# Optimization experiments

Measured on AMD Instinct MI355X. Metric: run time of the kernel, lower is better.

The kernel has to match this reference:

```python
import jax, jax.numpy as jnp
import numpy as np

D_STATE = 16
D_CONV = 4


def _ln_cf(x, w, b, eps=1e-6):
    # channels_first LayerNorm over dim 1 of (B,C,H,W)
    u = x.mean(1, keepdims=True)
    s = ((x - u) ** 2).mean(1, keepdims=True)
    return w[:, None, None] * ((x - u) / jnp.sqrt(s + eps)) + b[:, None, None]


def _ln_last(x, w, b, eps=1e-5):
    u = x.mean(-1, keepdims=True)
    s = ((x - u) ** 2).mean(-1, keepdims=True)
    return (x - u) / jnp.sqrt(s + eps) * w + b


def _mamba(xn, Win, convw, convb, Wx, Wdt, bdt, Alog, Dp):
    # xn: (B, L, d_model); returns (B, L, d_inner) (out_proj is Identity in this module)
    B, L, _ = xn.shape
    di = Win.shape[0] // 2
    xz = xn @ Win.T                                   # (B,L,2*di), in_proj bias=False
    xc, z = xz[..., :di], xz[..., di:]
    # causal depthwise conv1d along L (pad left d_conv-1, slice == torch pad+trim)
    xt = jnp.pad(xc.transpose(0, 2, 1), ((0, 0), (0, 0), (D_CONV - 1, 0)))
    xt = jax.lax.conv_general_dilated(xt, convw[:, None, :], (1,), 'VALID',
                                      dimension_numbers=('NCH', 'OIH', 'NCH'),
                                      feature_group_count=di)
    xs = jax.nn.silu(xt + convb[None, :, None]).transpose(0, 2, 1)  # (B,L,di)
    dtr = Wdt.shape[1]
    x_dbl = xs @ Wx.T                                 # (B,L,dtr+2*ds)
    dt = x_dbl[..., :dtr]
    Bm = x_dbl[..., dtr:dtr + D_STATE]                # (B,L,ds)
    Cm = x_dbl[..., dtr + D_STATE:]                   # (B,L,ds)
    delta = jax.nn.softplus(dt @ Wdt.T + bdt)         # (B,L,di)
    A = -jnp.exp(Alog)                                # (di,ds)
    dA = jnp.exp(delta[..., None] * A)                # (B,L,di,ds)
    dBx = delta[..., None] * Bm[:, :, None, :] * xs[..., None]

    def step(h, ab):
        a, b2 = ab
        h = a * h + b2
        return h, h

    h0 = jnp.zeros((B, di, D_STATE), xn.dtype)
    _, hs = jax.lax.scan(step, h0, (dA.transpose(1, 0, 2, 3), dBx.transpose(1, 0, 2, 3)))
    y = jnp.einsum('lbds,bls->bld', hs, Cm) + xs * Dp
    return y * jax.nn.silu(z)


def _dwconv2d(u, k, dil):
    c = k.shape[0]
    return jax.lax.conv_general_dilated(u, k[:, None], (1, 1),
                                        [(dil, dil), (dil, dil)],
                                        rhs_dilation=(dil, dil),
                                        dimension_numbers=('NCHW', 'OIHW', 'NCHW'),
                                        feature_group_count=c)


def _block(x, gamma1, gamma2, ln1_w, ln1_b, mn_w, mn_b,
           f_Win, f_convw, f_convb, f_Wx, f_Wdt, f_bdt, f_Alog, f_D,
           b_Win, b_convw, b_convb, b_Wx, b_Wdt, b_bdt, b_Alog, b_D,
           Wout, msff_win, msff_dw1, msff_dw2, msff_dw3, msff_wout):
    B, C, H, W = x.shape
    L = H * W
    # --- BiPixelMambaLayer branch ---
    x1 = _ln_cf(x, ln1_w, ln1_b)                       # norm1 (channels_first)
    xf = x1.reshape(B, C, L).transpose(0, 2, 1)        # (B,L,C)
    xn = _ln_last(xf, mn_w, mn_b)                      # inner nn.LayerNorm (eps=1e-5)
    yf = _mamba(xn, f_Win, f_convw, f_convb, f_Wx, f_Wdt, f_bdt, f_Alog, f_D)
    yb = _mamba(xn[:, ::-1], b_Win, b_convw, b_convb, b_Wx, b_Wdt, b_bdt, b_Alog, b_D)
    yo = (yf + yb[:, ::-1]) @ Wout.T                   # shared out_proj (bias=False)
    x = x + gamma1[:, None, None] * (yo.transpose(0, 2, 1).reshape(B, C, H, W) + x1)
    # --- MSFF branch (norm1 reused) ---
    inp = x
    xm = _ln_cf(x, ln1_w, ln1_b)
    h = jnp.einsum('oc,bchw->bohw', msff_win, xm)      # project_in (1x1x1 conv, depth=1)
    hid = msff_dw1.shape[0]
    h1 = _dwconv2d(h[:, :hid], msff_dw1, 1)            # Conv3d 3x3x3 w/ depth=1 == 2D center slice
    h2 = _dwconv2d(h[:, hid:2 * hid], msff_dw2, 2)
    h3 = _dwconv2d(h[:, 2 * hid:], msff_dw3, 3)
    g = jax.nn.gelu(h1, approximate=False) * h2 * h3
    xm = jnp.einsum('oc,bchw->bohw', msff_wout, g)     # project_out
    return inp + gamma2[:, None, None] * xm


def setup_inputs() -> dict:
    key = jax.random.key(0)
    ks = jax.random.split(key, 40)
    dim, di, dtr, ds, hid, Bn, H, W = 96, 192, 6, 16, 192, 2, 64, 64
    r = lambda i, shape, s=0.05: jax.random.normal(ks[i], shape, jnp.float32) * s
    inp = {
        'x': r(0, (Bn, dim, H, W), 1.0),
        'gamma1': r(1, (dim,), 0.1), 'gamma2': r(2, (dim,), 0.1),
        'ln1_w': 1.0 + r(3, (dim,), 0.1), 'ln1_b': r(4, (dim,), 0.1),
        'mn_w': 1.0 + r(5, (dim,), 0.1), 'mn_b': r(6, (dim,), 0.1),
    }
    i = 7
    for p in ('f_', 'b_'):
        inp[p + 'Win'] = r(i, (2 * di, dim)); i += 1
        inp[p + 'convw'] = r(i, (di, D_CONV), 0.2); i += 1
        inp[p + 'convb'] = r(i, (di,), 0.1); i += 1
        inp[p + 'Wx'] = r(i, (dtr + 2 * ds, di)); i += 1
        inp[p + 'Wdt'] = r(i, (di, dtr), 0.1); i += 1
        inp[p + 'bdt'] = r(i, (di,), 0.1); i += 1
        inp[p + 'Alog'] = jax.random.uniform(ks[i], (di, ds), jnp.float32, 0.0, 2.5); i += 1
        inp[p + 'D'] = r(i, (di,), 0.5); i += 1
    inp['Wout'] = r(i, (dim, di)); i += 1
    inp['msff_win'] = r(i, (3 * hid, dim)); i += 1
    inp['msff_dw1'] = r(i, (hid, 3, 3), 0.2); i += 1
    inp['msff_dw2'] = r(i, (hid, 3, 3), 0.2); i += 1
    inp['msff_dw3'] = r(i, (hid, 3, 3), 0.2); i += 1
    inp['msff_wout'] = r(i, (dim, hid)); i += 1
    return inp


def reference(x, gamma1, gamma2, ln1_w, ln1_b, mn_w, mn_b,
              f_Win, f_convw, f_convb, f_Wx, f_Wdt, f_bdt, f_Alog, f_D,
              b_Win, b_convw, b_convb, b_Wx, b_Wdt, b_bdt, b_Alog, b_D,
              Wout, msff_win, msff_dw1, msff_dw2, msff_dw3, msff_wout):
    return _block(x, gamma1, gamma2, ln1_w, ln1_b, mn_w, mn_b,
                  f_Win, f_convw, f_convb, f_Wx, f_Wdt, f_bdt, f_Alog, f_D,
                  b_Win, b_convw, b_convb, b_Wx, b_Wdt, b_bdt, b_Alog, b_D,
                  Wout, msff_win, msff_dw1, msff_dw2, msff_dw3, msff_wout)
```

## Files before the change

### kernel.cpp

```cpp
#include <hip/hip_runtime.h>
#include <hip/hip_bf16.h>
#include <math.h>

typedef __hip_bfloat16 bf16;
typedef _Float16 f16;
typedef f16  f16x8  __attribute__((ext_vector_type(8)));
typedef short short8 __attribute__((ext_vector_type(8)));
typedef unsigned short ushort8 __attribute__((ext_vector_type(8)));
typedef float floatx4 __attribute__((ext_vector_type(4)));

#define L_SEQ 4096
#define BATCH 2
#define DIM   96
#define DI    192
#define DS    16
#define HID   192
#define NPOS  (BATCH * L_SEQ)
#define NCH   512
#define CHUNK 8
#define GRP   32
#define NGRP  (NCH / GRP)
#define NREC  (2 * BATCH * DI)
#define LDBL  40
#define LOG2E 1.44269504088896f
#define TP    32

__device__ __forceinline__ float silu_f(float x) { return x / (1.f + __expf(-x)); }
__device__ __forceinline__ float softplus_f(float x) {
    return fmaxf(x, 0.f) + __logf(1.f + __expf(-fabsf(x)));
}
__device__ __forceinline__ float b2f(bf16 v) { return __bfloat162float(v); }
__device__ __forceinline__ float us2f(unsigned short u) {
    union { unsigned int i; float f; } cv; cv.i = ((unsigned int)u) << 16; return cv.f;
}

__global__ void k_prep(const float* __restrict__ fWin, const float* __restrict__ bWin,
                       const float* __restrict__ fWx,  const float* __restrict__ bWx,
                       const float* __restrict__ Wout, const float* __restrict__ mwin,
                       const float* __restrict__ mwout,
                       const float* __restrict__ fAlog, const float* __restrict__ bAlog,
                       const float* __restrict__ mdw1, const float* __restrict__ mdw2,
                       const float* __restrict__ mdw3,
                       bf16* __restrict__ war, float* __restrict__ a2tab,
                       float* __restrict__ mdwt) {
    int i = blockIdx.x * blockDim.x + threadIdx.x;
    if (i < 180480) {
        float v;
        if (i < 36864)        v = fWin[i];
        else if (i < 73728)   v = bWin[i - 36864];
        else if (i < 81024)   v = fWx[i - 73728];
        else if (i < 88320)   v = bWx[i - 81024];
        else if (i < 106752)  v = Wout[i - 88320];
        else if (i < 162048)  v = mwin[i - 106752];
        else                  v = mwout[i - 162048];
        war[i] = __float2bfloat16(v);
    } else if (i < 186624) {
        int j = i - 180480;
        int dir = j / 3072, rem = j % 3072;
        const float* al = dir ? bAlog : fAlog;
        a2tab[j] = -__expf(al[rem]) * LOG2E;
    } else if (i < 191808) {
        int j = i - 186624;
        int cv = j / 1728, rem = j % 1728;
        int tap = rem / 192, c = rem % 192;
        const float* src = (cv == 0) ? mdw1 : (cv == 1) ? mdw2 : mdw3;
        mdwt[j] = src[c * 9 + tap];
    }
}

__global__ void k_ln12_t(const float* __restrict__ x,
                         const float* __restrict__ ln1w, const float* __restrict__ ln1b,
                         const float* __restrict__ mnw,  const float* __restrict__ mnb,
                         bf16* __restrict__ XNbf) {
    __shared__ float xt[DIM][TP + 1];
    __shared__ float rs[8][TP], rss[8][TP];
    __shared__ float uu[TP], rr[TP];
    int p0 = blockIdx.x * TP;
    int b = p0 >> 12, l0 = p0 & (L_SEQ - 1);
    int t = threadIdx.x;
    int tg = t >> 5, li = t & 31;

    for (int idx = t; idx < DIM * TP; idx += 256) {
        int c = idx >> 5, q = idx & 31;
        xt[c][q] = x[((size_t)(b * DIM + c)) * L_SEQ + l0 + q];
    }
    __syncthreads();
    {
        float s = 0.f, ss = 0.f;
        for (int c = tg; c < DIM; c += 8) { float v = xt[c][li]; s += v; ss += v * v; }
        rs[tg][li] = s; rss[tg][li] = ss;
    }
    __syncthreads();
    if (t < TP) {
        float s = 0.f, ss = 0.f;
#pragma unroll
        for (int g = 0; g < 8; g++) { s += rs[g][t]; ss += rss[g][t]; }
        float u = s / DIM;
        uu[t] = u; rr[t] = rsqrtf(ss / DIM - u * u + 1e-6f);
    }
    __syncthreads();
    {
        float u = uu[li], r = rr[li];
        float s2 = 0.f, ss2 = 0.f;
        for (int c = tg; c < DIM; c += 8) {
            float tv = ln1w[c] * (xt[c][li] - u) * r + ln1b[c];
            xt[c][li] = tv;
            s2 += tv; ss2 += tv * tv;
        }
        rs[tg][li] = s2; rss[tg][li] = ss2;
    }
    __syncthreads();
    if (t < TP) {
        float s = 0.f, ss = 0.f;
#pragma unroll
        for (int g = 0; g < 8; g++) { s += rs[g][t]; ss += rss[g][t]; }
        float u = s / DIM;
        uu[t] = u; rr[t] = rsqrtf(ss / DIM - u * u + 1e-5f);
    }
    __syncthreads();
    for (int idx = t; idx < DIM * TP; idx += 256) {
        int q = idx / DIM, c = idx % DIM;
        XNbf[(size_t)(p0 + q) * DIM + c] =
            __float2bfloat16((xt[c][q] - uu[q]) * rr[q] * mnw[c] + mnb[c]);
    }
}

__global__ void mfma_nt_dir(const bf16* __restrict__ A0, const bf16* __restrict__ A1,
                            const bf16* __restrict__ W0, const bf16* __restrict__ W1,
                            void* __restrict__ C0, void* __restrict__ C1,
                            int M, int N, int K, int ldc, int pad6, int obf) {
    int z = blockIdx.z;
    const bf16* A = z ? A1 : A0;
    const bf16* W = z ? W1 : W0;
    void* C = z ? C1 : C0;
    int wave = threadIdx.x >> 6, lane = threadIdx.x & 63;
    int m0 = blockIdx.x * 64 + wave * 16;
    int n0 = blockIdx.y * 64;
    int lm = lane & 15, quad = lane >> 4;
    const short* Ap = (const short*)A + (size_t)(m0 + lm) * K + quad * 8;
    const short* Wp = (const short*)W;
    floatx4 acc[4];
#pragma unroll
    for (int t = 0; t < 4; t++) acc[t] = (floatx4){0.f, 0.f, 0.f, 0.f};
    for (int k0 = 0; k0 < K; k0 += 32) {
        short8 a = *(const short8*)(Ap + k0);
#pragma unroll
        for (int t = 0; t < 4; t++) {
            int n = n0 + t * 16 + lm;
            short8 b = (n < N) ? *(const short8*)(Wp + (size_t)n * K + k0 + quad * 8)
                               : (short8){0,0,0,0,0,0,0,0};
            acc[t] = __builtin_amdgcn_mfma_f32_16x16x32_bf16(a, b, acc[t], 0, 0, 0);
        }
    }
#pragma unroll
    for (int t = 0; t < 4; t++) {
        int n = n0 + t * 16 + lm;
        if (n < N) {
            int nn = (pad6 && n >= 6) ? n + 2 : n;
#pragma unroll
            for (int r = 0; r < 4; r++) {
                int m = m0 + quad * 4 + r;
                if (obf) ((bf16*)C)[(size_t)m * ldc + nn] = __float2bfloat16(acc[t][r]);
                else     ((float*)C)[(size_t)m * ldc + nn] = acc[t][r];
            }
        }
    }
}

__global__ void mfma_nt(const bf16* __restrict__ A, const bf16* __restrict__ W,
                        bf16* __restrict__ C, int M, int N, int K, int ldc) {
    int wave = threadIdx.x >> 6, lane = threadIdx.x & 63;
    int m0 = blockIdx.x * 64 + wave * 16;
    int n0 = blockIdx.y * 64;
    int lm = lane & 15, quad = lane >> 4;
    const short* Ap = (const short*)A + (size_t)(m0 + lm) * K + quad * 8;
    const short* Wp = (const short*)W;
    floatx4 acc[4];
#pragma unroll
    for (int t = 0; t < 4; t++) acc[t] = (floatx4){0.f, 0.f, 0.f, 0.f};
    for (int k0 = 0; k0 < K; k0 += 32) {
        short8 a = *(const short8*)(Ap + k0);
#pragma unroll
        for (int t = 0; t < 4; t++) {
            int n = n0 + t * 16 + lm;
            short8 b = (n < N) ? *(const short8*)(Wp + (size_t)n * K + k0 + quad * 8)
                               : (short8){0,0,0,0,0,0,0,0};
            acc[t] = __builtin_amdgcn_mfma_f32_16x16x32_bf16(a, b, acc[t], 0, 0, 0);
        }
    }
#pragma unroll
    for (int t = 0; t < 4; t++) {
        int n = n0 + t * 16 + lm;
        if (n < N) {
#pragma unroll
            for (int r = 0; r < 4; r++) {
                int m = m0 + quad * 4 + r;
                C[(size_t)m * ldc + n] = __float2bfloat16(acc[t][r]);
            }
        }
    }
}

__global__ void mfma_out(const bf16* __restrict__ Y1, const bf16* __restrict__ Y2,
                         const bf16* __restrict__ W, float* __restrict__ C,
                         int M, int N, int K, int ldc) {
    int wave = threadIdx.x >> 6, lane = threadIdx.x & 63;
    int m0 = blockIdx.x * 64 + wave * 16;
    int n0 = blockIdx.y * 64;
    int lm = lane & 15, quad = lane >> 4;
    const short* A1p = (const short*)Y1 + (size_t)(m0 + lm) * K + quad * 8;
    const short* A2p = (const short*)Y2 + (size_t)(m0 + lm) * K + quad * 8;
    const short* Wp  = (const short*)W;
    floatx4 acc[4];
#pragma unroll
    for (int t = 0; t < 4; t++) acc[t] = (floatx4){0.f, 0.f, 0.f, 0.f};
    for (int k0 = 0; k0 < K; k0 += 32) {
        short8 a1 = *(const short8*)(A1p + k0);
        short8 a2 = *(const short8*)(A2p + k0);
#pragma unroll
        for (int t = 0; t < 4; t++) {
            int n = n0 + t * 16 + lm;
            short8 b = (n < N) ? *(const short8*)(Wp + (size_t)n * K + k0 + quad * 8)
                               : (short8){0,0,0,0,0,0,0,0};
            acc[t] = __builtin_amdgcn_mfma_f32_16x16x32_bf16(a1, b, acc[t], 0, 0, 0);
            acc[t] = __builtin_amdgcn_mfma_f32_16x16x32_bf16(a2, b, acc[t], 0, 0, 0);
        }
    }
#pragma unroll
    for (int t = 0; t < 4; t++) {
        int n = n0 + t * 16 + lm;
        if (n < N) {
#pragma unroll
            for (int r = 0; r < 4; r++) {
                int m = m0 + quad * 4 + r;
                C[(size_t)m * ldc + n] = acc[t][r];
            }
        }
    }
}

__global__ void mfma_msffout(const bf16* __restrict__ A, const bf16* __restrict__ Bm,
                             const float* __restrict__ XMID, const float* __restrict__ gamma2,
                             float* __restrict__ out, int M, int K) {
    int wave = threadIdx.x >> 6, lane = threadIdx.x & 63;
    int m0 = blockIdx.x * 64 + wave * 16;
    int n0 = blockIdx.y * 64;
    int lm = lane & 15, quad = lane >> 4;
    int am = m0 + lm;
    bool aval = am < M;
    const short* Ap = (const short*)A + (size_t)am * K + quad * 8;
    const short* Bp = (const short*)Bm;
    floatx4 acc[4];
#pragma unroll
    for (int t = 0; t < 4; t++) acc[t] = (floatx4){0.f, 0.f, 0.f, 0.f};
    for (int k0 = 0; k0 < K; k0 += 32) {
        short8 a = aval ? *(const short8*)(Ap + k0) : (short8){0,0,0,0,0,0,0,0};
#pragma unroll
        for (int t = 0; t < 4; t++) {
            int n = n0 + t * 16 + lm;
            short8 b = *(const short8*)(Bp + (size_t)n * K + k0 + quad * 8);
            acc[t] = __builtin_amdgcn_mfma_f32_16x16x32_bf16(a, b, acc[t], 0, 0, 0);
        }
    }
#pragma unroll
    for (int t = 0; t < 4; t++) {
        int n = n0 + t * 16 + lm;
        int b = n >> 12, l = n & (L_SEQ - 1);
#pragma unroll
        for (int r = 0; r < 4; r++) {
            int m = m0 + quad * 4 + r;
            if (m < M) {
                size_t idx = ((size_t)(b * M + m)) * L_SEQ + l;
                out[idx] = XMID[idx] + gamma2[m] * acc[t][r];
            }
        }
    }
}

__global__ void k_conv_v(const bf16* __restrict__ XZF, const bf16* __restrict__ XZB,
                         const float* __restrict__ fw, const float* __restrict__ fb,
                         const float* __restrict__ bw, const float* __restrict__ bb,
                         bf16* __restrict__ XSF, bf16* __restrict__ XSB) {
    int dirb = blockIdx.y;
    int i = blockIdx.x * blockDim.x + threadIdx.x;
    int dg = i % 24;
    int p = i / 24;
    int b = p >> 12, l = p & (L_SEQ - 1);
    int d0 = dg * 8;
    const bf16* XZ = dirb ? XZB : XZF;
    const float* cw = dirb ? bw : fw;
    const float* cb = dirb ? bb : fb;

    float4 w[8];
#pragma unroll
    for (int j = 0; j < 8; j++) w[j] = *(const float4*)(cw + (d0 + j) * 4);
    float acc[8];
#pragma unroll
    for (int j = 0; j < 8; j++) acc[j] = cb[d0 + j];

#pragma unroll
    for (int k = 0; k < 4; k++) {
        int ls = dirb ? (l + 3 - k) : (l - 3 + k);
        if (ls >= 0 && ls < L_SEQ) {
            ushort8 xv = *(const ushort8*)((const unsigned short*)XZ +
                           ((size_t)(b * L_SEQ + ls)) * 384 + d0);
#pragma unroll
            for (int j = 0; j < 8; j++) {
                float wk = (k == 0) ? w[j].x : (k == 1) ? w[j].y : (k == 2) ? w[j].z : w[j].w;
                acc[j] += wk * us2f(xv[j]);
            }
        }
    }
    ushort8 ov;
#pragma unroll
    for (int j = 0; j < 8; j++) {
        bf16 t = __float2bfloat16(silu_f(acc[j]));
        ov[j] = *(unsigned short*)&t;
    }
    *(ushort8*)((unsigned short*)(dirb ? XSB : XSF) + (size_t)p * DI + d0) = ov;
}

__global__ void k_scan_p1(const float* __restrict__ DBLF, const float* __restrict__ DBLB,
                          const bf16* __restrict__ XSF,  const bf16* __restrict__ XSB,
                          const float* __restrict__ fWdt, const float* __restrict__ fbdt,
                          const float* __restrict__ bWdt, const float* __restrict__ bbdt,
                          const float* __restrict__ a2tab,
                          f16* __restrict__ P, f16* __restrict__ Q) {
    int t = blockIdx.x * blockDim.x + threadIdx.x;
    int d = t % DI;
    int g = t / DI;
    int chunk = g & (NCH - 1);
    int dirb = g >> 9;
    int b = dirb & 1, dir = dirb >> 1;

    const float* DBL = dir ? DBLB : DBLF;
    const bf16*  XS  = dir ? XSB  : XSF;
    const float* wdt = (dir ? bWdt : fWdt) + d * 6;
    float bdtv = (dir ? bbdt : fbdt)[d];

    float wd[6];
#pragma unroll
    for (int r = 0; r < 6; r++) wd[r] = wdt[r];
    const float* a2p = a2tab + (dir * DI + d) * 16;
    float A2[16], h[16];
#pragma unroll
    for (int v = 0; v < 4; v++) {
        float4 a2v = *(const float4*)(a2p + 4 * v);
        A2[4*v] = a2v.x; A2[4*v+1] = a2v.y; A2[4*v+2] = a2v.z; A2[4*v+3] = a2v.w;
    }
#pragma unroll
    for (int s = 0; s < 16; s++) h[s] = 0.f;

    int l = dir ? (L_SEQ - 1 - chunk * CHUNK) : chunk * CHUNK;
    int stp = dir ? -1 : 1;
    float sumdel = 0.f;

    for (int i = 0; i < CHUNK; i++) {
        size_t p = (size_t)b * L_SEQ + l;
        const float* row = DBL + p * LDBL;
        float dtv = bdtv;
#pragma unroll
        for (int r = 0; r < 6; r++) dtv += row[r] * wd[r];
        float del = softplus_f(dtv);
        float xs  = b2f(XS[p * DI + d]);
        const float4* bm = (const float4*)(row + 8);
        float4 B0 = bm[0], B1 = bm[1], B2 = bm[2], B3 = bm[3];
        float Bm[16] = {B0.x,B0.y,B0.z,B0.w, B1.x,B1.y,B1.z,B1.w,
                        B2.x,B2.y,B2.z,B2.w, B3.x,B3.y,B3.z,B3.w};
        float dx = del * xs;
        sumdel += del;
#pragma unroll
        for (int s = 0; s < 16; s++) {
            float dA = exp2f(del * A2[s]);
            h[s] = dA * h[s] + dx * Bm[s];
        }
        l += stp;
    }
    size_t idx = ((size_t)g * DI + d) * 16;
    f16x8 q0, q1, p0, p1;
#pragma unroll
    for (int j = 0; j < 8; j++) {
        q0[j] = (f16)h[j];
        q1[j] = (f16)h[8 + j];
        p0[j] = (f16)exp2f(A2[j] * sumdel);
        p1[j] = (f16)exp2f(A2[8 + j] * sumdel);
    }
    *(f16x8*)(Q + idx)     = q0;
    *(f16x8*)(Q + idx + 8) = q1;
    *(f16x8*)(P + idx)     = p0;
    *(f16x8*)(P + idx + 8) = p1;
}

__global__ void k_scan_p2a(const f16* __restrict__ P, const f16* __restrict__ Q,
                           float* __restrict__ Pg, float* __restrict__ Qg) {
    int t = blockIdx.x * blockDim.x + threadIdx.x;
    int s8 = t & 1;
    int d = (t >> 1) % DI;
    int rest = t / (DI * 2);
    int grp = rest % NGRP;
    int dirb = rest / NGRP;

    float Pr[8], Qr[8];
#pragma unroll
    for (int j = 0; j < 8; j++) { Pr[j] = 1.f; Qr[j] = 0.f; }

    size_t base = (((size_t)(dirb * NCH + grp * GRP)) * DI + d) * 16 + s8 * 8;
    for (int i = 0; i < GRP; i++) {
        size_t idx = base + (size_t)i * (DI * 16);
        f16x8 p8 = *(const f16x8*)(P + idx);
        f16x8 q8 = *(const f16x8*)(Q + idx);
#pragma unroll
        for (int j = 0; j < 8; j++) {
            float pv = (float)p8[j], qv = (float)q8[j];
            Qr[j] = pv * Qr[j] + qv;
            Pr[j] *= pv;
        }
    }
    size_t gidx = (((size_t)(dirb * NGRP + grp)) * DI + d) * 16 + s8 * 8;
#pragma unroll
    for (int v = 0; v < 2; v++) {
        *(float4*)(Pg + gidx + 4 * v) = make_float4(Pr[4*v], Pr[4*v+1], Pr[4*v+2], Pr[4*v+3]);
        *(float4*)(Qg + gidx + 4 * v) = make_float4(Qr[4*v], Qr[4*v+1], Qr[4*v+2], Qr[4*v+3]);
    }
}

__global__ void k_scan_p2b(const float* __restrict__ Pg, float* __restrict__ Qg) {
    int u = blockIdx.x * blockDim.x + threadIdx.x;
    int s = u & 15;
    int dd = (u >> 4) % DI;
    int dirb = u / (DI * 16);
    float runQ = 0.f;
#pragma unroll
    for (int g = 0; g < NGRP; g++) {
        size_t i = (((size_t)(dirb * NGRP + g)) * DI + dd) * 16 + s;
        float pg = Pg[i], qg = Qg[i];
        Qg[i] = runQ;
        runQ = pg * runQ + qg;
    }
}

__global__ void k_scan_p2c(const f16* __restrict__ P, f16* __restrict__ Q,
                           const float* __restrict__ Qg) {
    int t = blockIdx.x * blockDim.x + threadIdx.x;
    int s8 = t & 1;
    int d = (t >> 1) % DI;
    int rest = t / (DI * 2);
    int grp = rest % NGRP;
    int dirb = rest / NGRP;

    size_t gidx = (((size_t)(dirb * NGRP + grp)) * DI + d) * 16 + s8 * 8;
    float runQ[8];
#pragma unroll
    for (int v = 0; v < 2; v++) {
        float4 qv = *(const float4*)(Qg + gidx + 4 * v);
        runQ[4*v] = qv.x; runQ[4*v+1] = qv.y; runQ[4*v+2] = qv.z; runQ[4*v+3] = qv.w;
    }

    size_t base = (((size_t)(dirb * NCH + grp * GRP)) * DI + d) * 16 + s8 * 8;
    for (int i = 0; i < GRP; i++) {
        size_t idx = base + (size_t)i * (DI * 16);
        f16x8 p8 = *(const f16x8*)(P + idx);
        f16x8 q8 = *(const f16x8*)(Q + idx);
        f16x8 o8;
#pragma unroll
        for (int j = 0; j < 8; j++) {
            o8[j] = (f16)runQ[j];
            runQ[j] = (float)p8[j] * runQ[j] + (float)q8[j];
        }
        *(f16x8*)(Q + idx) = o8;
    }
}

__global__ void k_scan_p3(const float* __restrict__ DBLF, const float* __restrict__ DBLB,
                          const bf16* __restrict__ XSF,  const bf16* __restrict__ XSB,
                          const bf16* __restrict__ XZF,  const bf16* __restrict__ XZB,
                          const float* __restrict__ fWdt, const float* __restrict__ fbdt,
                          const float* __restrict__ bWdt, const float* __restrict__ bbdt,
                          const float* __restrict__ a2tab,
                          const float* __restrict__ fD,    const float* __restrict__ bD,
                          const f16* __restrict__ Q,
                          bf16* __restrict__ YSF, bf16* __restrict__ YSB) {
    int t = blockIdx.x * blockDim.x + threadIdx.x;
    int d = t % DI;
    int g = t / DI;
    int chunk = g & (NCH - 1);
    int dirb = g >> 9;
    int b = dirb & 1, dir = dirb >> 1;

    const float* DBL = dir ? DBLB : DBLF;
    const bf16*  XS  = dir ? XSB  : XSF;
    const bf16*  XZ  = dir ? XZB  : XZF;
    const float* wdt = (dir ? bWdt : fWdt) + d * 6;
    float bdtv = (dir ? bbdt : fbdt)[d];
    float Dp = dir ? bD[d] : fD[d];
    bf16* Y = dir ? YSB : YSF;

    float wd[6];
#pragma unroll
    for (int r = 0; r < 6; r++) wd[r] = wdt[r];
    const float* a2p = a2tab + (dir * DI + d) * 16;
    float A2[16], h[16];
#pragma unroll
    for (int v = 0; v < 4; v++) {
        float4 a2v = *(const float4*)(a2p + 4 * v);
        A2[4*v] = a2v.x; A2[4*v+1] = a2v.y; A2[4*v+2] = a2v.z; A2[4*v+3] = a2v.w;
    }
    size_t idx = ((size_t)g * DI + d) * 16;
    f16x8 q0 = *(const f16x8*)(Q + idx);
    f16x8 q1 = *(const f16x8*)(Q + idx + 8);
#pragma unroll
    for (int j = 0; j < 8; j++) { h[j] = (float)q0[j]; h[8 + j] = (float)q1[j]; }

    int l = dir ? (L_SEQ - 1 - chunk * CHUNK) : chunk * CHUNK;
    int stp = dir ? -1 : 1;

    for (int i = 0; i < CHUNK; i++) {
        size_t p = (size_t)b * L_SEQ + l;
        const float* row = DBL + p * LDBL;
        float dtv = bdtv;
#pragma unroll
        for (int r = 0; r < 6; r++) dtv += row[r] * wd[r];
        float del = softplus_f(dtv);
        float xs  = b2f(XS[p * DI + d]);
        float z   = b2f(XZ[p * 384 + 192 + d]);
        const float4* bm = (const float4*)(row + 8);
        float4 B0 = bm[0], B1 = bm[1], B2 = bm[2], B3 = bm[3];
        float4 C0 = bm[4], C1 = bm[5], C2 = bm[6], C3 = bm[7];
        float Bm[16] = {B0.x,B0.y,B0.z,B0.w, B1.x,B1.y,B1.z,B1.w,
                        B2.x,B2.y,B2.z,B2.w, B3.x,B3.y,B3.z,B3.w};
        float Cm[16] = {C0.x,C0.y,C0.z,C0.w, C1.x,C1.y,C1.z,C1.w,
                        C2.x,C2.y,C2.z,C2.w, C3.x,C3.y,C3.z,C3.w};
        float dx = del * xs;
        float pr = 0.f;
#pragma unroll
        for (int s = 0; s < 16; s++) {
            float dA = exp2f(del * A2[s]);
            h[s] = dA * h[s] + dx * Bm[s];
            pr += h[s] * Cm[s];
        }
        Y[p * DI + d] = __float2bfloat16((pr + xs * Dp) * silu_f(z));
        l += stp;
    }
}

__global__ void k_mid_t(const float* __restrict__ x, const float* __restrict__ YO,
                        const float* __restrict__ gamma1,
                        const float* __restrict__ ln1w, const float* __restrict__ ln1b,
                        float* __restrict__ XMID, bf16* __restrict__ XM2cl) {
    __shared__ float xt[DIM][TP + 1];
    __shared__ float yt[DIM][TP + 1];
    __shared__ float rs[8][TP], rss[8][TP];
    __shared__ float uu[TP], rr[TP];
    int p0 = blockIdx.x * TP;
    int b = p0 >> 12, l0 = p0 & (L_SEQ - 1);
    int t = threadIdx.x;
    int tg = t >> 5, li = t & 31;

    for (int idx = t; idx < DIM * TP; idx += 256) {
        int c = idx >> 5, q = idx & 31;
        xt[c][q] = x[((size_t)(b * DIM + c)) * L_SEQ + l0 + q];
    }
    for (int idx = t; idx < DIM * TP; idx += 256) {
        int q = idx / DIM, c = idx % DIM;
        yt[c][q] = YO[(size_t)(p0 + q) * DIM + c];
    }
    __syncthreads();
    {
        float s = 0.f, ss = 0.f;
        for (int c = tg; c < DIM; c += 8) { float v = xt[c][li]; s += v; ss += v * v; }
        rs[tg][li] = s; rss[tg][li] = ss;
    }
    __syncthreads();
    if (t < TP) {
        float s = 0.f, ss = 0.f;
#pragma unroll
        for (int g = 0; g < 8; g++) { s += rs[g][t]; ss += rss[g][t]; }
        float u = s / DIM;
        uu[t] = u; rr[t] = rsqrtf(ss / DIM - u * u + 1e-6f);
    }
    __syncthreads();
    {
        float u = uu[li], r = rr[li];
        float s = 0.f, ss = 0.f;
        for (int c = tg; c < DIM; c += 8) {
            float xv = xt[c][li];
            float x1 = ln1w[c] * (xv - u) * r + ln1b[c];
            float v = xv + gamma1[c] * (yt[c][li] + x1);
            XMID[((size_t)(b * DIM + c)) * L_SEQ + l0 + li] = v;
            xt[c][li] = v;
            s += v; ss += v * v;
        }
        rs[tg][li] = s; rss[tg][li] = ss;
    }
    __syncthreads();
    if (t < TP) {
        float s = 0.f, ss = 0.f;
#pragma unroll
        for (int g = 0; g < 8; g++) { s += rs[g][t]; ss += rss[g][t]; }
        float u = s / DIM;
        uu[t] = u; rr[t] = rsqrtf(ss / DIM - u * u + 1e-6f);
    }
    __syncthreads();
    for (int idx = t; idx < DIM * TP; idx += 256) {
        int q = idx / DIM, c = idx % DIM;
        XM2cl[(size_t)(p0 + q) * DIM + c] =
            __float2bfloat16(ln1w[c] * (xt[c][q] - uu[q]) * rr[q] + ln1b[c]);
    }
}

__global__ void k_msff_v(const bf16* __restrict__ H, const float* __restrict__ mdwt,
                         bf16* __restrict__ G) {
    int i = blockIdx.x * blockDim.x + threadIdx.x;
    int cg = i % 24;
    int p = i / 24;
    int c0 = cg * 8;
    int b = p >> 12, l = p & (L_SEQ - 1);
    int y = l >> 6, xc = l & 63;
    float a1[8] = {}, a2[8] = {}, a3[8] = {};
    const unsigned short* Hu = (const unsigned short*)H;

#pragma unroll
    for (int ky = 0; ky < 3; ky++) {
#pragma unroll
        for (int kx = 0; kx < 3; kx++) {
            int tap = ky * 3 + kx;
            {
                int y1 = y + (ky - 1), x1 = xc + (kx - 1);
                if (y1 >= 0 && y1 < 64 && x1 >= 0 && x1 < 64) {
                    float4 w0 = *(const float4*)(mdwt + tap * 192 + c0);
                    float4 w1 = *(const float4*)(mdwt + tap * 192 + c0 + 4);
                    ushort8 hv = *(const ushort8*)(Hu +
                        ((size_t)(b * L_SEQ + y1 * 64 + x1)) * 576 + c0);
                    float wv[8] = {w0.x,w0.y,w0.z,w0.w, w1.x,w1.y,w1.z,w1.w};
#pragma unroll
                    for (int j = 0; j < 8; j++) a1[j] += wv[j] * us2f(hv[j]);
                }
            }
            {
                int y2 = y + (ky - 1) * 2, x2 = xc + (kx - 1) * 2;
                if (y2 >= 0 && y2 < 64 && x2 >= 0 && x2 < 64) {
                    float4 w0 = *(const float4*)(mdwt + (9 + tap) * 192 + c0);
                    float4 w1 = *(const float4*)(mdwt + (9 + tap) * 192 + c0 + 4);
                    ushort8 hv = *(const ushort8*)(Hu +
                        ((size_t)(b * L_SEQ + y2 * 64 + x2)) * 576 + 192 + c0);
                    float wv[8] = {w0.x,w0.y,w0.z,w0.w, w1.x,w1.y,w1.z,w1.w};
#pragma unroll
                    for (int j = 0; j < 8; j++) a2[j] += wv[j] * us2f(hv[j]);
                }
            }
            {
                int y3 = y + (ky - 1) * 3, x3 = xc + (kx - 1) * 3;
                if (y3 >= 0 && y3 < 64 && x3 >= 0 && x3 < 64) {
                    float4 w0 = *(const float4*)(mdwt + (18 + tap) * 192 + c0);
                    float4 w1 = *(const float4*)(mdwt + (18 + tap) * 192 + c0 + 4);
                    ushort8 hv = *(const ushort8*)(Hu +
                        ((size_t)(b * L_SEQ + y3 * 64 + x3)) * 576 + 384 + c0);
                    float wv[8] = {w0.x,w0.y,w0.z,w0.w, w1.x,w1.y,w1.z,w1.w};
#pragma unroll
                    for (int j = 0; j < 8; j++) a3[j] += wv[j] * us2f(hv[j]);
                }
            }
        }
    }
    ushort8 ov;
#pragma unroll
    for (int j = 0; j < 8; j++) {
        float ge = 0.5f * a1[j] * (1.f + erff(a1[j] * 0.70710678118f));
        bf16 t = __float2bfloat16(ge * a2[j] * a3[j]);
        ov[j] = *(unsigned short*)&t;
    }
    *(ushort8*)((unsigned short*)G + (size_t)p * HID + c0) = ov;
}

extern "C" void kernel_launch(void* const* d_in, const int* in_sizes, int n_in,
                              void* d_out, int out_size, void* d_ws, size_t ws_size,
                              hipStream_t stream) {
    const float* x      = (const float*)d_in[0];
    const float* gamma1 = (const float*)d_in[1];
    const float* gamma2 = (const float*)d_in[2];
    const float* ln1w   = (const float*)d_in[3];
    const float* ln1b   = (const float*)d_in[4];
    const float* mnw    = (const float*)d_in[5];
    const float* mnb    = (const float*)d_in[6];
    const float* fWin   = (const float*)d_in[7];
    const float* fconvw = (const float*)d_in[8];
    const float* fconvb = (const float*)d_in[9];
    const float* fWx    = (const float*)d_in[10];
    const float* fWdt   = (const float*)d_in[11];
    const float* fbdt   = (const float*)d_in[12];
    const float* fAlog  = (const float*)d_in[13];
    const float* fD     = (const float*)d_in[14];
    const float* bWin   = (const float*)d_in[15];
    const float* bconvw = (const float*)d_in[16];
    const float* bconvb = (const float*)d_in[17];
    const float* bWx    = (const float*)d_in[18];
    const float* bWdt   = (const float*)d_in[19];
    const float* bbdt   = (const float*)d_in[20];
    const float* bAlog  = (const float*)d_in[21];
    const float* bD     = (const float*)d_in[22];
    const float* Wout   = (const float*)d_in[23];
    const float* mwin   = (const float*)d_in[24];
    const float* mdw1   = (const float*)d_in[25];
    const float* mdw2   = (const float*)d_in[26];
    const float* mdw3   = (const float*)d_in[27];
    const float* mwout  = (const float*)d_in[28];
    float* out = (float*)d_out;

    float* ws = (float*)d_ws;
    bf16*  XNbf  = (bf16*)(ws);
    bf16*  XZF   = (bf16*)(ws + 393216);
    bf16*  XZB   = (bf16*)(ws + 1966080);
    bf16*  XSF   = (bf16*)(ws + 3538944);
    bf16*  XSB   = (bf16*)(ws + 4325376);
    float* DBLF  = ws + 5111808;
    float* DBLB  = ws + 5439488;
    f16*   Ph    = (f16*)(ws + 5767168);
    f16*   Qh    = (f16*)(ws + 8912896);
    bf16*  YSFbf = (bf16*)(ws + 12058624);
    bf16*  YSBbf = (bf16*)(ws + 12845056);
    float* YO    = ws + 13631488;
    float* XMID  = ws + 14417920;
    bf16*  XM2cl = (bf16*)(ws + 15204352);
    bf16*  Hcl   = (bf16*)(ws + 15597568);
    bf16*  Gcl   = (bf16*)(ws + 17956864);
    bf16*  WAR   = (bf16*)(ws + 18743296);
    float* A2tab = ws + 18833536;
    float* MDWT  = ws + 18839680;
    float* Pgb   = ws + 18844864;
    float* Qgb   = ws + 19041472;

    const bf16* fWinB  = WAR;
    const bf16* bWinB  = WAR + 36864;
    const bf16* fWxB   = WAR + 73728;
    const bf16* bWxB   = WAR + 81024;
    const bf16* WoutB  = WAR + 88320;
    const bf16* mwinB  = WAR + 106752;
    const bf16* mwoutB = WAR + 162048;

    k_prep<<<750, 256, 0, stream>>>(fWin, bWin, fWx, bWx, Wout, mwin, mwout,
                                    fAlog, bAlog, mdw1, mdw2, mdw3,
                                    WAR, A2tab, MDWT);
    k_ln12_t<<<NPOS / TP, 256, 0, stream>>>(x, ln1w, ln1b, mnw, mnb, XNbf);
    mfma_nt_dir<<<dim3(128, 6, 2), 256, 0, stream>>>(XNbf, XNbf, fWinB, bWinB,
                                                     XZF, XZB, NPOS, 384, DIM, 384, 0, 1);
    k_conv_v<<<dim3(NPOS * 24 / 256, 2), 256, 0, stream>>>(XZF, XZB, fconvw, fconvb,
                                                           bconvw, bconvb, XSF, XSB);
    mfma_nt_dir<<<dim3(128, 1, 2), 256, 0, stream>>>(XSF, XSB, fWxB, bWxB,
                                                     DBLF, DBLB, NPOS, 38, DI, LDBL, 1, 0);
    k_scan_p1<<<NREC * NCH / 256, 256, 0, stream>>>(DBLF, DBLB, XSF, XSB,
                                                    fWdt, fbdt, bWdt, bbdt,
                                                    A2tab, Ph, Qh);
    k_scan_p2a<<<4 * NGRP * DI * 2 / 256, 256, 0, stream>>>(Ph, Qh, Pgb, Qgb);
    k_scan_p2b<<<NREC * 16 / 256, 256, 0, stream>>>(Pgb, Qgb);
    k_scan_p2c<<<4 * NGRP * DI * 2 / 256, 256, 0, stream>>>(Ph, Qh, Qgb);
    k_scan_p3<<<NREC * NCH / 256, 256, 0, stream>>>(DBLF, DBLB, XSF, XSB, XZF, XZB,
                                                    fWdt, fbdt, bWdt, bbdt,
                                                    A2tab, fD, bD, Qh,
                                                    YSFbf, YSBbf);
    mfma_out<<<dim3(128, 2), 256, 0, stream>>>(YSFbf, YSBbf, WoutB, YO, NPOS, DIM, DI, DIM);
    k_mid_t<<<NPOS / TP, 256, 0, stream>>>(x, YO, gamma1, ln1w, ln1b, XMID, XM2cl);
    mfma_nt<<<dim3(128, 9), 256, 0, stream>>>(XM2cl, mwinB, Hcl, NPOS, 576, DIM, 576);
    k_msff_v<<<NPOS * 24 / 256, 256, 0, stream>>>(Hcl, MDWT, Gcl);
    mfma_msffout<<<dim3(2, 128), 256, 0, stream>>>(mwoutB, Gcl, XMID, gamma2, out, DIM, HID);
}
```

Baseline: 287.7 us.

## Fuse chunk scan with in-block group combine and merge prep into layernorm

The chunked selective scan is restructured: chunks become longer (16 steps, 256 chunks). Each block now combines its group of chunk summaries in shared memory and writes the exclusive prefix P/Q plus the group totals directly. This replaces the separate p2a and p2c passes. Phase 3 then rebuilds each chunk's initial state as Pexc*Qg+Qexc, and the weight-prep kernel is merged into the layernorm launch as extra blocks. The aim is fewer launches and less global round-tripping of chunk summaries, at the cost of longer serial chunks, reduced parallelism in p1/p3, and an extra f16 rounding of the exclusive products.

Result: faster. 269.6 us (-6.3%).

```diff
diff --git a/kernel.cpp b/kernel.cpp
--- a/kernel.cpp
+++ b/kernel.cpp
@@ -16,12 +16,13 @@
 #define DS    16
 #define HID   192
 #define NPOS  (BATCH * L_SEQ)
-#define NCH   512
-#define CHUNK 8
-#define GRP   32
+#define NCH   256
+#define CHUNK 16
+#define GRP   16
 #define NGRP  (NCH / GRP)
 #define NREC  (2 * BATCH * DI)
 #define LDBL  40
+#define PLANE (4 * NCH * DI * 8)
 #define LOG2E 1.44269504088896f
 #define TP    32
 
@@ -34,47 +35,48 @@
     union { unsigned int i; float f; } cv; cv.i = ((unsigned int)u) << 16; return cv.f;
 }
 
-__global__ void k_prep(const float* __restrict__ fWin, const float* __restrict__ bWin,
-                       const float* __restrict__ fWx,  const float* __restrict__ bWx,
-                       const float* __restrict__ Wout, const float* __restrict__ mwin,
-                       const float* __restrict__ mwout,
-                       const float* __restrict__ fAlog, const float* __restrict__ bAlog,
-                       const float* __restrict__ mdw1, const float* __restrict__ mdw2,
-                       const float* __restrict__ mdw3,
-                       bf16* __restrict__ war, float* __restrict__ a2tab,
-                       float* __restrict__ mdwt) {
-    int i = blockIdx.x * blockDim.x + threadIdx.x;
-    if (i < 180480) {
-        float v;
-        if (i < 36864)        v = fWin[i];
-        else if (i < 73728)   v = bWin[i - 36864];
-        else if (i < 81024)   v = fWx[i - 73728];
-        else if (i < 88320)   v = bWx[i - 81024];
-        else if (i < 106752)  v = Wout[i - 88320];
-        else if (i < 162048)  v = mwin[i - 106752];
-        else                  v = mwout[i - 162048];
-        war[i] = __float2bfloat16(v);
-    } else if (i < 186624) {
-        int j = i - 180480;
-        int dir = j / 3072, rem = j % 3072;
-        const float* al = dir ? bAlog : fAlog;
-        a2tab[j] = -__expf(al[rem]) * LOG2E;
-    } else if (i < 191808) {
-        int j = i - 186624;
-        int cv = j / 1728, rem = j % 1728;
-        int tap = rem / 192, c = rem % 192;
-        const float* src = (cv == 0) ? mdw1 : (cv == 1) ? mdw2 : mdw3;
-        mdwt[j] = src[c * 9 + tap];
-    }
-}
-
-__global__ void k_ln12_t(const float* __restrict__ x,
-                         const float* __restrict__ ln1w, const float* __restrict__ ln1b,
-                         const float* __restrict__ mnw,  const float* __restrict__ mnb,
-                         bf16* __restrict__ XNbf) {
+__global__ void k_ln12_prep(const float* __restrict__ x,
+                            const float* __restrict__ ln1w, const float* __restrict__ ln1b,
+                            const float* __restrict__ mnw,  const float* __restrict__ mnb,
+                            bf16* __restrict__ XNbf,
+                            const float* __restrict__ fWin, const float* __restrict__ bWin,
+                            const float* __restrict__ fWx,  const float* __restrict__ bWx,
+                            const float* __restrict__ Wout, const float* __restrict__ mwin,
+                            const float* __restrict__ mwout,
+                            const float* __restrict__ fAlog, const float* __restrict__ bAlog,
+                            const float* __restrict__ mdw1, const float* __restrict__ mdw2,
+                            const float* __restrict__ mdw3,
+                            bf16* __restrict__ war, float* __restrict__ a2tab,
+                            float* __restrict__ mdwt) {
     __shared__ float xt[DIM][TP + 1];
     __shared__ float rs[8][TP], rss[8][TP];
     __shared__ float uu[TP], rr[TP];
+    if (blockIdx.x >= NPOS / TP) {
+        int i = (blockIdx.x - NPOS / TP) * 256 + threadIdx.x;
+        if (i < 180480) {
+            float v;
+            if (i < 36864)        v = fWin[i];
+            else if (i < 73728)   v = bWin[i - 36864];
+            else if (i < 81024)   v = fWx[i - 73728];
+            else if (i < 88320)   v = bWx[i - 81024];
+            else if (i < 106752)  v = Wout[i - 88320];
+            else if (i < 162048)  v = mwin[i - 106752];
+            else                  v = mwout[i - 162048];
+            war[i] = __float2bfloat16(v);
+        } else if (i < 186624) {
+            int j = i - 180480;
+            int dir = j / 3072, rem = j % 3072;
+            const float* al = dir ? bAlog : fAlog;
+            a2tab[j] = -__expf(al[rem]) * LOG2E;
+        } else if (i < 191808) {
+            int j = i - 186624;
+            int cv = j / 1728, rem = j % 1728;
+            int tap = rem / 192, c = rem % 192;
+            const float* src = (cv == 0) ? mdw1 : (cv == 1) ? mdw2 : mdw3;
+            mdwt[j] = src[c * 9 + tap];
+        }
+        return;
+    }
     int p0 = blockIdx.x * TP;
     int b = p0 >> 12, l0 = p0 & (L_SEQ - 1);
     int t = threadIdx.x;
@@ -320,18 +322,21 @@
     *(ushort8*)((unsigned short*)(dirb ? XSB : XSF) + (size_t)p * DI + d0) = ov;
 }
 
-__global__ void k_scan_p1(const float* __restrict__ DBLF, const float* __restrict__ DBLB,
-                          const bf16* __restrict__ XSF,  const bf16* __restrict__ XSB,
-                          const float* __restrict__ fWdt, const float* __restrict__ fbdt,
-                          const float* __restrict__ bWdt, const float* __restrict__ bbdt,
-                          const float* __restrict__ a2tab,
-                          f16* __restrict__ P, f16* __restrict__ Q) {
-    int t = blockIdx.x * blockDim.x + threadIdx.x;
-    int d = t % DI;
-    int g = t / DI;
-    int chunk = g & (NCH - 1);
-    int dirb = g >> 9;
+__global__ void k_scan_p1g(const float* __restrict__ DBLF, const float* __restrict__ DBLB,
+                           const bf16* __restrict__ XSF,  const bf16* __restrict__ XSB,
+                           const float* __restrict__ fWdt, const float* __restrict__ fbdt,
+                           const float* __restrict__ bWdt, const float* __restrict__ bbdt,
+                           const float* __restrict__ a2tab,
+                           f16* __restrict__ Pexc, f16* __restrict__ Qexc,
+                           float* __restrict__ Pg, float* __restrict__ Qg) {
+    __shared__ f16x8 Pl[2][GRP][16];
+    __shared__ f16x8 Ql[2][GRP][16];
+    int dsl = blockIdx.x, grp = blockIdx.y, dirb = blockIdx.z;
+    int t = threadIdx.x;
+    int chunk = t >> 4, dl = t & 15;
+    int d = dsl * 16 + dl;
     int b = dirb & 1, dir = dirb >> 1;
+    int gc = grp * GRP + chunk;
 
     const float* DBL = dir ? DBLB : DBLF;
     const bf16*  XS  = dir ? XSB  : XSF;
@@ -351,7 +356,7 @@
 #pragma unroll
     for (int s = 0; s < 16; s++) h[s] = 0.f;
 
-    int l = dir ? (L_SEQ - 1 - chunk * CHUNK) : chunk * CHUNK;
+    int l = dir ? (L_SEQ - 1 - gc * CHUNK) : gc * CHUNK;
     int stp = dir ? -1 : 1;
     float sumdel = 0.f;
 
@@ -376,51 +381,48 @@
         }
         l += stp;
     }
-    size_t idx = ((size_t)g * DI + d) * 16;
-    f16x8 q0, q1, p0, p1;
-#pragma unroll
-    for (int j = 0; j < 8; j++) {
-        q0[j] = (f16)h[j];
-        q1[j] = (f16)h[8 + j];
-        p0[j] = (f16)exp2f(A2[j] * sumdel);
-        p1[j] = (f16)exp2f(A2[8 + j] * sumdel);
-    }
-    *(f16x8*)(Q + idx)     = q0;
-    *(f16x8*)(Q + idx + 8) = q1;
-    *(f16x8*)(P + idx)     = p0;
-    *(f16x8*)(P + idx + 8) = p1;
-}
-
-__global__ void k_scan_p2a(const f16* __restrict__ P, const f16* __restrict__ Q,
-                           float* __restrict__ Pg, float* __restrict__ Qg) {
-    int t = blockIdx.x * blockDim.x + threadIdx.x;
-    int s8 = t & 1;
-    int d = (t >> 1) % DI;
-    int rest = t / (DI * 2);
-    int grp = rest % NGRP;
-    int dirb = rest / NGRP;
-
-    float Pr[8], Qr[8];
-#pragma unroll
-    for (int j = 0; j < 8; j++) { Pr[j] = 1.f; Qr[j] = 0.f; }
-
-    size_t base = (((size_t)(dirb * NCH + grp * GRP)) * DI + d) * 16 + s8 * 8;
-    for (int i = 0; i < GRP; i++) {
-        size_t idx = base + (size_t)i * (DI * 16);
-        f16x8 p8 = *(const f16x8*)(P + idx);
-        f16x8 q8 = *(const f16x8*)(Q + idx);
+    {
+        f16x8 p0, p1, q0, q1;
 #pragma unroll
         for (int j = 0; j < 8; j++) {
-            float pv = (float)p8[j], qv = (float)q8[j];
-            Qr[j] = pv * Qr[j] + qv;
-            Pr[j] *= pv;
-        }
-    }
-    size_t gidx = (((size_t)(dirb * NGRP + grp)) * DI + d) * 16 + s8 * 8;
-#pragma unroll
-    for (int v = 0; v < 2; v++) {
-        *(float4*)(Pg + gidx + 4 * v) = make_float4(Pr[4*v], Pr[4*v+1], Pr[4*v+2], Pr[4*v+3]);
-        *(float4*)(Qg + gidx + 4 * v) = make_float4(Qr[4*v], Qr[4*v+1], Qr[4*v+2], Qr[4*v+3]);
+            q0[j] = (f16)h[j];
+            q1[j] = (f16)h[8 + j];
+            p0[j] = (f16)exp2f(A2[j] * sumdel);
+            p1[j] = (f16)exp2f(A2[8 + j] * sumdel);
+        }
+        Pl[0][chunk][dl] = p0; Pl[1][chunk][dl] = p1;
+        Ql[0][chunk][dl] = q0; Ql[1][chunk][dl] = q1;
+    }
+    __syncthreads();
+
+    {
+        int s  = t & 15, dl2 = t >> 4;
+        int s8 = s >> 3, sl = s & 7;
+        f16* Pp = (f16*)&Pl[s8][0][dl2];
+        f16* Qp = (f16*)&Ql[s8][0][dl2];
+        float runP = 1.f, runQ = 0.f;
+#pragma unroll
+        for (int c = 0; c < GRP; c++) {
+            float pv = (float)Pp[c * 128 + sl];
+            float qv = (float)Qp[c * 128 + sl];
+            Pp[c * 128 + sl] = (f16)runP;
+            Qp[c * 128 + sl] = (f16)runQ;
+            runQ = pv * runQ + qv;
+            runP *= pv;
+        }
+        int d2 = dsl * 16 + dl2;
+        size_t gidx = (((size_t)(dirb * NGRP + grp)) * DI + d2) * 16 + s;
+        Pg[gidx] = runP;
+        Qg[gidx] = runQ;
+    }
+    __syncthreads();
+
+    {
+        size_t base = ((size_t)(dirb * NCH + gc) * DI + d) * 8;
+        *(f16x8*)(Pexc + base)         = Pl[0][chunk][dl];
+        *(f16x8*)(Pexc + PLANE + base) = Pl[1][chunk][dl];
+        *(f16x8*)(Qexc + base)         = Ql[0][chunk][dl];
+        *(f16x8*)(Qexc + PLANE + base) = Ql[1][chunk][dl];
     }
 }
 
@@ -439,52 +441,22 @@
     }
 }
 
-__global__ void k_scan_p2c(const f16* __restrict__ P, f16* __restrict__ Q,
-                           const float* __restrict__ Qg) {
-    int t = blockIdx.x * blockDim.x + threadIdx.x;
-    int s8 = t & 1;
-    int d = (t >> 1) % DI;
-    int rest = t / (DI * 2);
-    int grp = rest % NGRP;
-    int dirb = rest / NGRP;
-
-    size_t gidx = (((size_t)(dirb * NGRP + grp)) * DI + d) * 16 + s8 * 8;
-    float runQ[8];
-#pragma unroll
-    for (int v = 0; v < 2; v++) {
-        float4 qv = *(const float4*)(Qg + gidx + 4 * v);
-        runQ[4*v] = qv.x; runQ[4*v+1] = qv.y; runQ[4*v+2] = qv.z; runQ[4*v+3] = qv.w;
-    }
-
-    size_t base = (((size_t)(dirb * NCH + grp * GRP)) * DI + d) * 16 + s8 * 8;
-    for (int i = 0; i < GRP; i++) {
-        size_t idx = base + (size_t)i * (DI * 16);
-        f16x8 p8 = *(const f16x8*)(P + idx);
-        f16x8 q8 = *(const f16x8*)(Q + idx);
-        f16x8 o8;
-#pragma unroll
-        for (int j = 0; j < 8; j++) {
-            o8[j] = (f16)runQ[j];
-            runQ[j] = (float)p8[j] * runQ[j] + (float)q8[j];
-        }
-        *(f16x8*)(Q + idx) = o8;
-    }
-}
-
-__global__ void k_scan_p3(const float* __restrict__ DBLF, const float* __restrict__ DBLB,
-                          const bf16* __restrict__ XSF,  const bf16* __restrict__ XSB,
-                          const bf16* __restrict__ XZF,  const bf16* __restrict__ XZB,
-                          const float* __restrict__ fWdt, const float* __restrict__ fbdt,
-                          const float* __restrict__ bWdt, const float* __restrict__ bbdt,
-                          const float* __restrict__ a2tab,
-                          const float* __restrict__ fD,    const float* __restrict__ bD,
-                          const f16* __restrict__ Q,
-                          bf16* __restrict__ YSF, bf16* __restrict__ YSB) {
+__global__ void k_scan_p3g(const float* __restrict__ DBLF, const float* __restrict__ DBLB,
+                           const bf16* __restrict__ XSF,  const bf16* __restrict__ XSB,
+                           const bf16* __restrict__ XZF,  const bf16* __restrict__ XZB,
+                           const float* __restrict__ fWdt, const float* __restrict__ fbdt,
+                           const float* __restrict__ bWdt, const float* __restrict__ bbdt,
+                           const float* __restrict__ a2tab,
+                           const float* __restrict__ fD,    const float* __restrict__ bD,
+                           const f16* __restrict__ Pexc, const f16* __restrict__ Qexc,
+                           const float* __restrict__ Qg,
+                           bf16* __restrict__ YSF, bf16* __restrict__ YSB) {
     int t = blockIdx.x * blockDim.x + threadIdx.x;
     int d = t % DI;
     int g = t / DI;
-    int chunk = g & (NCH - 1);
-    int dirb = g >> 9;
+    int gch = g & (NCH - 1);
+    int dirb = g >> 8;
+    int grp = gch >> 4;
     int b = dirb & 1, dir = dirb >> 1;
 
     const float* DBL = dir ? DBLB : DBLF;
@@ -505,13 +477,27 @@
         float4 a2v = *(const float4*)(a2p + 4 * v);
         A2[4*v] = a2v.x; A2[4*v+1] = a2v.y; A2[4*v+2] = a2v.z; A2[4*v+3] = a2v.w;
     }
-    size_t idx = ((size_t)g * DI + d) * 16;
-    f16x8 q0 = *(const f16x8*)(Q + idx);
-    f16x8 q1 = *(const f16x8*)(Q + idx + 8);
-#pragma unroll
-    for (int j = 0; j < 8; j++) { h[j] = (float)q0[j]; h[8 + j] = (float)q1[j]; }
-
-    int l = dir ? (L_SEQ - 1 - chunk * CHUNK) : chunk * CHUNK;
+    {
+        size_t base = ((size_t)g * DI + d) * 8;
+        f16x8 pe0 = *(const f16x8*)(Pexc + base);
+        f16x8 pe1 = *(const f16x8*)(Pexc + PLANE + base);
+        f16x8 qe0 = *(const f16x8*)(Qexc + base);
+        f16x8 qe1 = *(const f16x8*)(Qexc + PLANE + base);
+        size_t gidx = (((size_t)(dirb * NGRP + grp)) * DI + d) * 16;
+        float qg[16];
+#pragma unroll
+        for (int v = 0; v < 4; v++) {
+            float4 qv = *(const float4*)(Qg + gidx + 4 * v);
+            qg[4*v] = qv.x; qg[4*v+1] = qv.y; qg[4*v+2] = qv.z; qg[4*v+3] = qv.w;
+        }
+#pragma unroll
+        for (int j = 0; j < 8; j++) {
+            h[j]     = (float)pe0[j] * qg[j]     + (float)qe0[j];
+            h[8 + j] = (float)pe1[j] * qg[8 + j] + (float)qe1[j];
+        }
+    }
+
+    int l = dir ? (L_SEQ - 1 - gch * CHUNK) : gch * CHUNK;
     int stp = dir ? -1 : 1;
 
     for (int i = 0; i < CHUNK; i++) {
@@ -737,26 +723,24 @@
     const bf16* mwinB  = WAR + 106752;
     const bf16* mwoutB = WAR + 162048;
 
-    k_prep<<<750, 256, 0, stream>>>(fWin, bWin, fWx, bWx, Wout, mwin, mwout,
-                                    fAlog, bAlog, mdw1, mdw2, mdw3,
-                                    WAR, A2tab, MDWT);
-    k_ln12_t<<<NPOS / TP, 256, 0, stream>>>(x, ln1w, ln1b, mnw, mnb, XNbf);
+    k_ln12_prep<<<NPOS / TP + 750, 256, 0, stream>>>(x, ln1w, ln1b, mnw, mnb, XNbf,
+                                                     fWin, bWin, fWx, bWx, Wout, mwin, mwout,
+                                                     fAlog, bAlog, mdw1, mdw2, mdw3,
+                                                     WAR, A2tab, MDWT);
     mfma_nt_dir<<<dim3(128, 6, 2), 256, 0, stream>>>(XNbf, XNbf, fWinB, bWinB,
                                                      XZF, XZB, NPOS, 384, DIM, 384, 0, 1);
     k_conv_v<<<dim3(NPOS * 24 / 256, 2), 256, 0, stream>>>(XZF, XZB, fconvw, fconvb,
                                                            bconvw, bconvb, XSF, XSB);
     mfma_nt_dir<<<dim3(128, 1, 2), 256, 0, stream>>>(XSF, XSB, fWxB, bWxB,
                                                      DBLF, DBLB, NPOS, 38, DI, LDBL, 1, 0);
-    k_scan_p1<<<NREC * NCH / 256, 256, 0, stream>>>(DBLF, DBLB, XSF, XSB,
-                                                    fWdt, fbdt, bWdt, bbdt,
-                                                    A2tab, Ph, Qh);
-    k_scan_p2a<<<4 * NGRP * DI * 2 / 256, 256, 0, stream>>>(Ph, Qh, Pgb, Qgb);
+    k_scan_p1g<<<dim3(DI / 16, NGRP, 4), 256, 0, stream>>>(DBLF, DBLB, XSF, XSB,
+                                                           fWdt, fbdt, bWdt, bbdt,
+                                                           A2tab, Ph, Qh, Pgb, Qgb);
     k_scan_p2b<<<NREC * 16 / 256, 256, 0, stream>>>(Pgb, Qgb);
-    k_scan_p2c<<<4 * NGRP * DI * 2 / 256, 256, 0, stream>>>(Ph, Qh, Qgb);
-    k_scan_p3<<<NREC * NCH / 256, 256, 0, stream>>>(DBLF, DBLB, XSF, XSB, XZF, XZB,
-                                                    fWdt, fbdt, bWdt, bbdt,
-                                                    A2tab, fD, bD, Qh,
-                                                    YSFbf, YSBbf);
+    k_scan_p3g<<<4 * NCH * DI / 256, 256, 0, stream>>>(DBLF, DBLB, XSF, XSB, XZF, XZB,
+                                                       fWdt, fbdt, bWdt, bbdt,
+                                                       A2tab, fD, bD, Ph, Qh, Qgb,
+                                                       YSFbf, YSBbf);
     mfma_out<<<dim3(128, 2), 256, 0, stream>>>(YSFbf, YSBbf, WoutB, YO, NPOS, DIM, DI, DIM);
     k_mid_t<<<NPOS / TP, 256, 0, stream>>>(x, YO, gamma1, ln1w, ln1b, XMID, XM2cl);
     mfma_nt<<<dim3(128, 9), 256, 0, stream>>>(XM2cl, mwinB, Hcl, NPOS, 576, DIM, 576);
```
